# Optimization experiments

Hardware: AMD Instinct MI355X
Metric: run time of the kernel (lower is better)

## Reference

```python
import math
import jax, jax.numpy as jnp
import numpy as np

N_HEADS = 8
GROUPS = 32
EPS = 1e-5


def setup_inputs() -> dict:
    key = jax.random.key(0)
    ks = jax.random.split(key, 4)
    B, C, H, W = 8, 512, 32, 32
    x = jax.random.normal(ks[0], (B, C, H, W), dtype=jnp.float32)
    gn_scale = jnp.ones((C,), dtype=jnp.float32)
    gn_bias = jnp.zeros((C,), dtype=jnp.float32)
    # small init so softmax logits stay in a sane range (original zero-inits
    # proj_out; we use small random weights so the output is non-trivial)
    qkv_w = jax.random.normal(ks[1], (3 * C, C), dtype=jnp.float32) * 0.02
    qkv_b = jnp.zeros((3 * C,), dtype=jnp.float32)
    proj_w = jax.random.normal(ks[2], (C, C), dtype=jnp.float32) * 0.02
    proj_b = jnp.zeros((C,), dtype=jnp.float32)
    return {"x": x, "gn_scale": gn_scale, "gn_bias": gn_bias,
            "qkv_w": qkv_w, "qkv_b": qkv_b,
            "proj_w": proj_w, "proj_b": proj_b}


def reference(x, gn_scale, gn_bias, qkv_w, qkv_b, proj_w, proj_b):
    b, c, H, W = x.shape
    L = H * W
    xr = x.reshape(b, c, L)

    # GroupNorm32: normalize in fp32 over (channels_per_group, L)
    xf = xr.astype(jnp.float32).reshape(b, GROUPS, -1)
    mu = xf.mean(axis=-1, keepdims=True)
    var = xf.var(axis=-1, keepdims=True)
    xn = ((xf - mu) * jax.lax.rsqrt(var + EPS)).reshape(b, c, L)
    xn = (xn * gn_scale[:, None] + gn_bias[:, None]).astype(x.dtype)

    # 1x1 conv QKV projection: [b, 3C, L]
    qkv = jnp.einsum('oc,bcl->bol', qkv_w, xn) + qkv_b[:, None]

    # QKVAttentionLegacy: split 3C axis as (heads, 3*ch)
    ch = c // N_HEADS
    qkv = qkv.reshape(b * N_HEADS, 3 * ch, L)
    q, k, v = qkv[:, :ch], qkv[:, ch:2 * ch], qkv[:, 2 * ch:]
    scale = 1.0 / math.sqrt(math.sqrt(ch))
    w = jnp.einsum('bct,bcs->bts', q * scale, k * scale)  # [b*h, L, L]
    w = jax.nn.softmax(w.astype(jnp.float32), axis=-1).astype(qkv.dtype)
    a = jnp.einsum('bts,bcs->bct', w, v).reshape(b, c, L)

    # 1x1 conv output projection + residual
    h = jnp.einsum('oc,bcl->bol', proj_w, a) + proj_b[:, None]
    return (xr + h).reshape(b, c, H, W)
```

## Files before the change

### kernel.cpp

```cpp
#include <hip/hip_runtime.h>
#include <hip/hip_bf16.h>

typedef __attribute__((ext_vector_type(8))) short v8s;
typedef __attribute__((ext_vector_type(8))) unsigned short u16x8;
typedef __attribute__((ext_vector_type(4))) float v4f;
typedef __attribute__((ext_vector_type(16))) float f32x16;

#define MFMA16(a, b, c) __builtin_amdgcn_mfma_f32_16x16x32_bf16((a), (b), (c), 0, 0, 0)
#define MFMA32(a, b, c) __builtin_amdgcn_mfma_f32_32x32x16_bf16((a), (b), (c), 0, 0, 0)

#define GLL16(g, l)                                                        \
  __builtin_amdgcn_global_load_lds(                                        \
      (const __attribute__((address_space(1))) unsigned int*)(g),          \
      (__attribute__((address_space(3))) unsigned int*)(l), 16, 0, 0)

#if __has_builtin(__builtin_amdgcn_exp2f)
__device__ __forceinline__ float exp2n(float x) { return __builtin_amdgcn_exp2f(x); }
#else
__device__ __forceinline__ float exp2n(float x) {
  float r; asm("v_exp_f32 %0, %1" : "=v"(r) : "v"(x)); return r;
}
#endif

__device__ __forceinline__ unsigned short f2bf(float f) {
  union { float f; unsigned u; } v; v.f = f;
  unsigned r = v.u + 0x7fffu + ((v.u >> 16) & 1u);
  return (unsigned short)(r >> 16);
}

__device__ __forceinline__ unsigned cvtpk(float lo, float hi) {
  unsigned r;
  asm("v_cvt_pk_bf16_f32 %0, %1, %2" : "=v"(r) : "v"(lo), "v"(hi));
  return r;
}
__device__ __forceinline__ void pl32swap(unsigned& a, unsigned& b) {
  asm("v_permlane32_swap_b32 %0, %1" : "+v"(a), "+v"(b));
}

__global__ __launch_bounds__(256) void cvt_gn_kernel(const float* __restrict__ in0,
                                                     unsigned short* __restrict__ out0,
                                                     const float* __restrict__ in1,
                                                     unsigned short* __restrict__ out1,
                                                     int n0, int n1,
                                                     const float* __restrict__ x,
                                                     const float* __restrict__ gsc,
                                                     const float* __restrict__ gbi,
                                                     unsigned short* __restrict__ xnT) {
  __shared__ __align__(16) float xsf[16384];
  if (blockIdx.x < 1024) {
    int i = blockIdx.x * 256 + threadIdx.x;
    const float* in; unsigned short* out;
    if (i < n0) { in = in0; out = out0; }
    else        { i -= n0; if (i >= n1) return; in = in1; out = out1; }
    float4 v = ((const float4*)in)[i];
    ushort4 o;
    o.x = f2bf(v.x); o.y = f2bf(v.y); o.z = f2bf(v.z); o.w = f2bf(v.w);
    ((ushort4*)out)[i] = o;
    return;
  }
  const int bg = blockIdx.x - 1024;
  const int b = bg >> 5, g = bg & 31;
  const int tid = threadIdx.x;
  const float4* xp4 = (const float4*)(x + (size_t)bg * 16384);
  float4* xs4 = (float4*)xsf;
  float s = 0.f, ss = 0.f;
  #pragma unroll
  for (int k = 0; k < 16; ++k) {
    const int i = k * 256 + tid;
    float4 v = xp4[i];
    xs4[i] = v;
    s  += (v.x + v.y) + (v.z + v.w);
    ss += (v.x * v.x + v.y * v.y) + (v.z * v.z + v.w * v.w);
  }
  #pragma unroll
  for (int d = 1; d < 64; d <<= 1) { s += __shfl_xor(s, d); ss += __shfl_xor(ss, d); }
  __syncthreads();
  float save = 0.f;
  if (tid < 10) save = xsf[tid];
  __syncthreads();
  if ((tid & 63) == 0) { xsf[(tid >> 6) * 2] = s; xsf[(tid >> 6) * 2 + 1] = ss; }
  __syncthreads();
  if (tid == 0) {
    const float S  = xsf[0] + xsf[2] + xsf[4] + xsf[6];
    const float SS = xsf[1] + xsf[3] + xsf[5] + xsf[7];
    const float mu  = S * (1.f / 16384.f);
    const float var = SS * (1.f / 16384.f) - mu * mu;
    xsf[8] = mu; xsf[9] = rsqrtf(var + 1e-5f);
  }
  __syncthreads();
  const float mu = xsf[8], rs = xsf[9];
  __syncthreads();
  if (tid < 10) xsf[tid] = save;
  __syncthreads();
  float scv[16], biv[16];
  #pragma unroll
  for (int j = 0; j < 16; ++j) {
    scv[j] = gsc[g * 16 + j] * rs;
    biv[j] = gbi[g * 16 + j] - mu * scv[j];
  }
  unsigned short* dp = xnT + (size_t)b * 1024 * 512 + g * 16;
  #pragma unroll
  for (int k = 0; k < 4; ++k) {
    const int l = k * 256 + tid;
    u16x8 o0, o1;
    #pragma unroll
    for (int j = 0; j < 8; ++j) o0[j] = f2bf(xsf[j * 1024 + l] * scv[j] + biv[j]);
    #pragma unroll
    for (int j = 0; j < 8; ++j) o1[j] = f2bf(xsf[(8 + j) * 1024 + l] * scv[8 + j] + biv[8 + j]);
    *(u16x8*)(dp + (size_t)l * 512)     = o0;
    *(u16x8*)(dp + (size_t)l * 512 + 8) = o1;
  }
}

template <bool QKV, int NT>
__global__ __launch_bounds__(256) void gemm_kernel(
    const unsigned short* __restrict__ A,
    const unsigned short* __restrict__ BT,
    const float* __restrict__ bias,
    const float* __restrict__ xres,
    float* __restrict__ outf,
    unsigned short* __restrict__ qT,
    unsigned short* __restrict__ kT,
    unsigned short* __restrict__ vO) {
  constexpr int K = 512;
  constexpr int NFR = NT / 32;
  constexpr int NJOB = 16 + NT / 8;
  const int n0 = blockIdx.x * NT, m0 = blockIdx.y * 128, b = blockIdx.z;
  const unsigned short* Bp = BT + (size_t)b * 1024 * K;

  __shared__ __align__(16) unsigned short As[128][64];
  __shared__ __align__(16) unsigned short Bs[NT][64];

  const int tid = threadIdx.x, lane = tid & 63, w = tid >> 6;
  const int quad = lane >> 4, l15 = lane & 15;
  const int wm = (w >> 1) * 64, wn = (w & 1) * (NT / 2);
  const int srow = lane >> 3;
  const int scol = ((lane & 7) ^ srow) * 8;
  const int ck0 = ((quad ^ (l15 & 7)) * 8);
  const int ck1 = ck0 ^ 32;
  const unsigned short* Asf = &As[0][0];
  const unsigned short* Bsf = &Bs[0][0];

  v4f acc[4][NFR];
  #pragma unroll
  for (int i = 0; i < 4; ++i)
    #pragma unroll
    for (int j = 0; j < NFR; ++j) acc[i][j] = (v4f){0.f, 0.f, 0.f, 0.f};

  for (int kk = 0; kk < K; kk += 64) {
    __syncthreads();
    #pragma unroll
    for (int jj = 0; jj < NJOB / 4; ++jj) {
      const int job = w * (NJOB / 4) + jj;
      if (job < 16) {
        GLL16(A + (size_t)(m0 + job * 8 + srow) * K + kk + scol, &As[job * 8][0]);
      } else {
        const int j2 = job - 16;
        GLL16(Bp + (size_t)(n0 + j2 * 8 + srow) * K + kk + scol, &Bs[j2 * 8][0]);
      }
    }
    __syncthreads();
    #pragma unroll
    for (int h = 0; h < 2; ++h) {
      const int ck = h ? ck1 : ck0;
      v8s af[4], bf[NFR];
      #pragma unroll
      for (int mt = 0; mt < 4; ++mt) af[mt] = *(const v8s*)(Asf + (wm + mt * 16 + l15) * 64 + ck);
      #pragma unroll
      for (int nt = 0; nt < NFR; ++nt) bf[nt] = *(const v8s*)(Bsf + (wn + nt * 16 + l15) * 64 + ck);
      #pragma unroll
      for (int mt = 0; mt < 4; ++mt)
        #pragma unroll
        for (int nt = 0; nt < NFR; ++nt)
          acc[mt][nt] = MFMA16(af[mt], bf[nt], acc[mt][nt]);
    }
  }

  if (QKV) {
    const int bh8 = b * 8;
    const float cs = 0.18033688011112042f;
    #pragma unroll
    for (int mt = 0; mt < 4; ++mt) {
      const int m4 = m0 + wm + mt * 16 + quad * 4;
      const int h = m4 / 192;
      const int rr = m4 - h * 192;
      const int part = rr >> 6;
      const int ch = rr & 63;
      const float b0 = bias[m4], b1 = bias[m4 + 1], b2 = bias[m4 + 2], b3 = bias[m4 + 3];
      #pragma unroll
      for (int nt = 0; nt < NFR; ++nt) {
        const int n = n0 + wn + nt * 16 + l15;
        v4f a = acc[mt][nt];
        const float v0 = a[0] + b0, v1 = a[1] + b1, v2 = a[2] + b2, v3 = a[3] + b3;
        if (part == 0) {
          ushort4 st4;
          st4.x = f2bf(v0 * cs); st4.y = f2bf(v1 * cs);
          st4.z = f2bf(v2 * cs); st4.w = f2bf(v3 * cs);
          *(ushort4*)(qT + ((size_t)(bh8 + h) * 1024 + n) * 64 + ch) = st4;
        } else if (part == 1) {
          ushort4 st4;
          st4.x = f2bf(v0); st4.y = f2bf(v1); st4.z = f2bf(v2); st4.w = f2bf(v3);
          *(ushort4*)(kT + ((size_t)(bh8 + h) * 1024 + n) * 64 + ch) = st4;
        } else {
          unsigned short* dp = vO + ((size_t)(bh8 + h) * 64 + ch) * 1024 + n;
          dp[0] = f2bf(v0); dp[1024] = f2bf(v1); dp[2048] = f2bf(v2); dp[3072] = f2bf(v3);
        }
      }
    }
  } else {
    #pragma unroll
    for (int mt = 0; mt < 4; ++mt) {
      const int m4 = m0 + wm + mt * 16 + quad * 4;
      const float b0 = bias[m4], b1 = bias[m4 + 1], b2 = bias[m4 + 2], b3 = bias[m4 + 3];
      #pragma unroll
      for (int nt = 0; nt < NFR; ++nt) {
        const int n = n0 + wn + nt * 16 + l15;
        const size_t i0 = ((size_t)b * 512 + m4) * 1024 + n;
        outf[i0]        = xres[i0]        + acc[mt][nt][0] + b0;
        outf[i0 + 1024] = xres[i0 + 1024] + acc[mt][nt][1] + b1;
        outf[i0 + 2048] = xres[i0 + 2048] + acc[mt][nt][2] + b2;
        outf[i0 + 3072] = xres[i0 + 3072] + acc[mt][nt][3] + b3;
      }
    }
  }
}

__global__ __launch_bounds__(256) void attn_kernel(const unsigned short* __restrict__ qT,
                                                   const unsigned short* __restrict__ kT,
                                                   const unsigned short* __restrict__ vv,
                                                   unsigned short* __restrict__ aT) {
  const int bh = blockIdx.x;
  const int t0 = blockIdx.y * 128;
  const unsigned short* qb = qT + (size_t)bh * 1024 * 64;
  const unsigned short* kb = kT + (size_t)bh * 1024 * 64;
  const unsigned short* vb = vv + (size_t)bh * 64 * 1024;

  __shared__ __align__(16) unsigned short Ks[2][128][64];
  __shared__ __align__(16) unsigned short Vs[2][2][64][64];

  const int tid = threadIdx.x, w = tid >> 6, lane = tid & 63;
  const int l31 = lane & 31, h = lane >> 5;
  const int srow = lane >> 3;
  const int scol = ((lane & 7) ^ srow) * 8;

  #pragma unroll
  for (int jj = 0; jj < 4; ++jj) {
    const int seg = w * 4 + jj;
    GLL16(qb + (size_t)(t0 + seg * 8 + srow) * 64 + scol, &Ks[0][0][0] + seg * 8 * 64);
  }
  __syncthreads();
  v8s qf[4];
  {
    const int row = w * 32 + l31;
    const unsigned short* qr = &Ks[0][0][0] + row * 64;
    const int rx = row & 7;
    #pragma unroll
    for (int kb2 = 0; kb2 < 4; ++kb2)
      qf[kb2] = *(const v8s*)(qr + ((kb2 * 2 + h) ^ rx) * 8);
  }
  __syncthreads();

  #pragma unroll
  for (int jj = 0; jj < 8; ++jj) {
    const int j = w * 8 + jj;
    if (j < 16) {
      GLL16(kb + (size_t)(j * 8 + srow) * 64 + scol, &Ks[0][j * 8][0]);
    } else {
      const int j2 = j - 16, hf = j2 >> 3, cg = (j2 & 7) * 8;
      GLL16(vb + (size_t)(cg + srow) * 1024 + hf * 64 + scol, &Vs[0][hf][cg][0]);
    }
  }

  f32x16 o[2];
  #pragma unroll
  for (int cb = 0; cb < 2; ++cb)
    #pragma unroll
    for (int r = 0; r < 16; ++r) o[cb][r] = 0.f;
  float lsum = 0.f;

  for (int it = 0; it < 8; ++it) {
    __syncthreads();
    if (it + 1 < 8) {
      const int s1 = (it + 1) * 128, bp1 = (it + 1) & 1;
      #pragma unroll
      for (int jj = 0; jj < 8; ++jj) {
        const int j = w * 8 + jj;
        if (j < 16) {
          GLL16(kb + (size_t)(s1 + j * 8 + srow) * 64 + scol, &Ks[bp1][j * 8][0]);
        } else {
          const int j2 = j - 16, hf = j2 >> 3, cg = (j2 & 7) * 8;
          GLL16(vb + (size_t)(cg + srow) * 1024 + s1 + hf * 64 + scol,
                &Vs[bp1][hf][cg][0]);
        }
      }
    }
    const int buf = it & 1;

    #pragma unroll
    for (int hf = 0; hf < 2; ++hf) {
      const unsigned short* Kb = &Ks[buf][hf * 64][0];
      const unsigned short* Vb = &Vs[buf][hf][0][0];

      v8s kf[2][4], vf[2][4];
      #pragma unroll
      for (int sb = 0; sb < 2; ++sb) {
        const int row = sb * 32 + l31, rx = row & 7;
        const unsigned short* kr = Kb + row * 64;
        #pragma unroll
        for (int kb2 = 0; kb2 < 4; ++kb2)
          kf[sb][kb2] = *(const v8s*)(kr + ((kb2 * 2 + h) ^ rx) * 8);
      }
      #pragma unroll
      for (int cb = 0; cb < 2; ++cb) {
        const int row = cb * 32 + l31, rx = row & 7;
        const unsigned short* vr = Vb + row * 64;
        #pragma unroll
        for (int i = 0; i < 4; ++i)
          vf[cb][i] = *(const v8s*)(vr + ((i * 2 + h) ^ rx) * 8);
      }

      #pragma unroll
      for (int sb = 0; sb < 2; ++sb) {
        f32x16 sa = {0.f,0.f,0.f,0.f,0.f,0.f,0.f,0.f,0.f,0.f,0.f,0.f,0.f,0.f,0.f,0.f};
        #pragma unroll
        for (int kb2 = 0; kb2 < 4; ++kb2)
          sa = MFMA32(kf[sb][kb2], qf[kb2], sa);
        float p[16]; float rsum = 0.f;
        #pragma unroll
        for (int r = 0; r < 16; ++r) { p[r] = exp2n(sa[r]); rsum += p[r]; }
        lsum += rsum;
        unsigned c0 = cvtpk(p[0], p[1]),  c1 = cvtpk(p[2], p[3]);
        unsigned c2 = cvtpk(p[4], p[5]),  c3 = cvtpk(p[6], p[7]);
        pl32swap(c0, c2); pl32swap(c1, c3);
        unsigned c4 = cvtpk(p[8], p[9]),  c5 = cvtpk(p[10], p[11]);
        unsigned c6 = cvtpk(p[12], p[13]), c7 = cvtpk(p[14], p[15]);
        pl32swap(c4, c6); pl32swap(c5, c7);
        union { v8s v; unsigned u[4]; } pa0, pa1;
        pa0.u[0] = c0; pa0.u[1] = c1; pa0.u[2] = c2; pa0.u[3] = c3;
        pa1.u[0] = c4; pa1.u[1] = c5; pa1.u[2] = c6; pa1.u[3] = c7;
        #pragma unroll
        for (int cb = 0; cb < 2; ++cb) {
          o[cb] = MFMA32(pa0.v, vf[cb][sb * 2 + 0], o[cb]);
          o[cb] = MFMA32(pa1.v, vf[cb][sb * 2 + 1], o[cb]);
        }
      }
    }
  }

  const int b = bh >> 3, hd = bh & 7;
  lsum += __shfl_xor(lsum, 32);
  #pragma unroll
  for (int r = 0; r < 16; ++r) {
    const int trow = (r & 3) + 8 * (r >> 2) + 4 * h;
    const float inv = 1.0f / __shfl(lsum, trow);
    const int t = t0 + w * 32 + trow;
    unsigned short* dst = aT + ((size_t)b * 1024 + t) * 512 + hd * 64;
    dst[l31]      = f2bf(o[0][r] * inv);
    dst[32 + l31] = f2bf(o[1][r] * inv);
  }
}

extern "C" void kernel_launch(void* const* d_in, const int* in_sizes, int n_in,
                              void* d_out, int out_size, void* d_ws, size_t ws_size,
                              hipStream_t stream) {
  const float* x    = (const float*)d_in[0];
  const float* gsc  = (const float*)d_in[1];
  const float* gbi  = (const float*)d_in[2];
  const float* qkvw = (const float*)d_in[3];
  const float* qkvb = (const float*)d_in[4];
  const float* pjw  = (const float*)d_in[5];
  const float* pjb  = (const float*)d_in[6];
  float* out = (float*)d_out;

  unsigned short* ws  = (unsigned short*)d_ws;
  unsigned short* qw  = ws;
  unsigned short* pw  = qw + 786432;
  unsigned short* xnT = pw + 262144 + 1024;
  unsigned short* qT  = xnT + 4194304;
  unsigned short* kT  = qT + 4194304;
  unsigned short* vv  = kT + 4194304;
  unsigned short* aT  = vv + 4194304;

  cvt_gn_kernel<<<dim3(1280), dim3(256), 0, stream>>>(qkvw, qw, pjw, pw, 196608, 65536,
                                                      x, gsc, gbi, xnT);
  gemm_kernel<true, 128><<<dim3(8, 12, 8), dim3(256), 0, stream>>>(
      qw, xnT, qkvb, nullptr, nullptr, qT, kT, vv);
  attn_kernel<<<dim3(64, 8), dim3(256), 0, stream>>>(qT, kT, vv, aT);
  gemm_kernel<false, 64><<<dim3(16, 4, 8), dim3(256), 0, stream>>>(
      pw, aT, pjb, x, out, nullptr, nullptr, nullptr);
}
```

Baseline: 142.5 us.

## Use 512-thread attention blocks with a 4-slot LDS ring and 3-deep prefetch

The attention kernel now runs 8 waves per block covering 256 query rows, so each K/V tile loaded into LDS is shared by twice as many query rows. The K/V stream moves from a double buffer of 128-key tiles to a 4-slot ring of 64-key tiles, prefetched three tiles ahead. Explicit vmcnt waits and raw s_barriers replace __syncthreads. This aims to hide global-load latency and halve K/V traffic per query, at the cost of fewer blocks (256) on the device and hand-tuned wait counts that must match the number of loads issued per wave.

```diff
diff --git a/kernel.cpp b/kernel.cpp
--- a/kernel.cpp
+++ b/kernel.cpp
@@ -225,18 +225,17 @@
   }
 }
 
-__global__ __launch_bounds__(256) void attn_kernel(const unsigned short* __restrict__ qT,
+__global__ __launch_bounds__(512) void attn_kernel(const unsigned short* __restrict__ qT,
                                                    const unsigned short* __restrict__ kT,
                                                    const unsigned short* __restrict__ vv,
                                                    unsigned short* __restrict__ aT) {
   const int bh = blockIdx.x;
-  const int t0 = blockIdx.y * 128;
+  const int t0 = blockIdx.y * 256;
   const unsigned short* qb = qT + (size_t)bh * 1024 * 64;
   const unsigned short* kb = kT + (size_t)bh * 1024 * 64;
   const unsigned short* vb = vv + (size_t)bh * 64 * 1024;
 
-  __shared__ __align__(16) unsigned short Ks[2][128][64];
-  __shared__ __align__(16) unsigned short Vs[2][2][64][64];
+  __shared__ __align__(16) unsigned short ring[4][2][64][64];
 
   const int tid = threadIdx.x, w = tid >> 6, lane = tid & 63;
   const int l31 = lane & 31, h = lane >> 5;
@@ -246,13 +245,13 @@
   #pragma unroll
   for (int jj = 0; jj < 4; ++jj) {
     const int seg = w * 4 + jj;
-    GLL16(qb + (size_t)(t0 + seg * 8 + srow) * 64 + scol, &Ks[0][0][0] + seg * 8 * 64);
+    GLL16(qb + (size_t)(t0 + seg * 8 + srow) * 64 + scol, &ring[0][0][0][0] + seg * 8 * 64);
   }
   __syncthreads();
   v8s qf[4];
   {
     const int row = w * 32 + l31;
-    const unsigned short* qr = &Ks[0][0][0] + row * 64;
+    const unsigned short* qr = &ring[0][0][0][0] + row * 64;
     const int rx = row & 7;
     #pragma unroll
     for (int kb2 = 0; kb2 < 4; ++kb2)
@@ -261,13 +260,17 @@
   __syncthreads();
 
   #pragma unroll
-  for (int jj = 0; jj < 8; ++jj) {
-    const int j = w * 8 + jj;
-    if (j < 16) {
-      GLL16(kb + (size_t)(j * 8 + srow) * 64 + scol, &Ks[0][j * 8][0]);
-    } else {
-      const int j2 = j - 16, hf = j2 >> 3, cg = (j2 & 7) * 8;
-      GLL16(vb + (size_t)(cg + srow) * 1024 + hf * 64 + scol, &Vs[0][hf][cg][0]);
+  for (int tt = 0; tt < 3; ++tt) {
+    const int s1 = tt * 64;
+    #pragma unroll
+    for (int jj = 0; jj < 2; ++jj) {
+      if (w < 4) {
+        const int rg = (w * 2 + jj) * 8;
+        GLL16(kb + (size_t)(s1 + rg + srow) * 64 + scol, &ring[tt][0][rg][0]);
+      } else {
+        const int cg = ((w - 4) * 2 + jj) * 8;
+        GLL16(vb + (size_t)(cg + srow) * 1024 + s1 + scol, &ring[tt][1][cg][0]);
+      }
     }
   }
 
@@ -278,71 +281,73 @@
     for (int r = 0; r < 16; ++r) o[cb][r] = 0.f;
   float lsum = 0.f;
 
-  for (int it = 0; it < 8; ++it) {
-    __syncthreads();
-    if (it + 1 < 8) {
-      const int s1 = (it + 1) * 128, bp1 = (it + 1) & 1;
-      #pragma unroll
-      for (int jj = 0; jj < 8; ++jj) {
-        const int j = w * 8 + jj;
-        if (j < 16) {
-          GLL16(kb + (size_t)(s1 + j * 8 + srow) * 64 + scol, &Ks[bp1][j * 8][0]);
+  #pragma unroll
+  for (int t = 0; t < 16; ++t) {
+    asm volatile("s_barrier" ::: "memory");
+    if (t + 3 < 16) {
+      const int s1 = (t + 3) * 64, sl = (t + 3) & 3;
+      #pragma unroll
+      for (int jj = 0; jj < 2; ++jj) {
+        if (w < 4) {
+          const int rg = (w * 2 + jj) * 8;
+          GLL16(kb + (size_t)(s1 + rg + srow) * 64 + scol, &ring[sl][0][rg][0]);
         } else {
-          const int j2 = j - 16, hf = j2 >> 3, cg = (j2 & 7) * 8;
-          GLL16(vb + (size_t)(cg + srow) * 1024 + s1 + hf * 64 + scol,
-                &Vs[bp1][hf][cg][0]);
+          const int cg = ((w - 4) * 2 + jj) * 8;
+          GLL16(vb + (size_t)(cg + srow) * 1024 + s1 + scol, &ring[sl][1][cg][0]);
         }
       }
     }
-    const int buf = it & 1;
-
-    #pragma unroll
-    for (int hf = 0; hf < 2; ++hf) {
-      const unsigned short* Kb = &Ks[buf][hf * 64][0];
-      const unsigned short* Vb = &Vs[buf][hf][0][0];
-
-      v8s kf[2][4], vf[2][4];
-      #pragma unroll
-      for (int sb = 0; sb < 2; ++sb) {
-        const int row = sb * 32 + l31, rx = row & 7;
-        const unsigned short* kr = Kb + row * 64;
-        #pragma unroll
-        for (int kb2 = 0; kb2 < 4; ++kb2)
-          kf[sb][kb2] = *(const v8s*)(kr + ((kb2 * 2 + h) ^ rx) * 8);
-      }
+    if (t < 13)       asm volatile("s_waitcnt vmcnt(6)" ::: "memory");
+    else if (t == 13) asm volatile("s_waitcnt vmcnt(4)" ::: "memory");
+    else if (t == 14) asm volatile("s_waitcnt vmcnt(2)" ::: "memory");
+    else              asm volatile("s_waitcnt vmcnt(0)" ::: "memory");
+    asm volatile("s_barrier" ::: "memory");
+
+    const int sl = t & 3;
+    const unsigned short* Kb = &ring[sl][0][0][0];
+    const unsigned short* Vb = &ring[sl][1][0][0];
+
+    v8s kf[2][4], vf[2][4];
+    #pragma unroll
+    for (int sb = 0; sb < 2; ++sb) {
+      const int row = sb * 32 + l31, rx = row & 7;
+      const unsigned short* kr = Kb + row * 64;
+      #pragma unroll
+      for (int kb2 = 0; kb2 < 4; ++kb2)
+        kf[sb][kb2] = *(const v8s*)(kr + ((kb2 * 2 + h) ^ rx) * 8);
+    }
+    #pragma unroll
+    for (int cb = 0; cb < 2; ++cb) {
+      const int row = cb * 32 + l31, rx = row & 7;
+      const unsigned short* vr = Vb + row * 64;
+      #pragma unroll
+      for (int i = 0; i < 4; ++i)
+        vf[cb][i] = *(const v8s*)(vr + ((i * 2 + h) ^ rx) * 8);
+    }
+
+    #pragma unroll
+    for (int sb = 0; sb < 2; ++sb) {
+      f32x16 sa = {0.f,0.f,0.f,0.f,0.f,0.f,0.f,0.f,0.f,0.f,0.f,0.f,0.f,0.f,0.f,0.f};
+      #pragma unroll
+      for (int kb2 = 0; kb2 < 4; ++kb2)
+        sa = MFMA32(kf[sb][kb2], qf[kb2], sa);
+      float p[16]; float rsum = 0.f;
+      #pragma unroll
+      for (int r = 0; r < 16; ++r) { p[r] = exp2n(sa[r]); rsum += p[r]; }
+      lsum += rsum;
+      unsigned c0 = cvtpk(p[0], p[1]),  c1 = cvtpk(p[2], p[3]);
+      unsigned c2 = cvtpk(p[4], p[5]),  c3 = cvtpk(p[6], p[7]);
+      pl32swap(c0, c2); pl32swap(c1, c3);
+      unsigned c4 = cvtpk(p[8], p[9]),  c5 = cvtpk(p[10], p[11]);
+      unsigned c6 = cvtpk(p[12], p[13]), c7 = cvtpk(p[14], p[15]);
+      pl32swap(c4, c6); pl32swap(c5, c7);
+      union { v8s v; unsigned u[4]; } pa0, pa1;
+      pa0.u[0] = c0; pa0.u[1] = c1; pa0.u[2] = c2; pa0.u[3] = c3;
+      pa1.u[0] = c4; pa1.u[1] = c5; pa1.u[2] = c6; pa1.u[3] = c7;
       #pragma unroll
       for (int cb = 0; cb < 2; ++cb) {
-        const int row = cb * 32 + l31, rx = row & 7;
-        const unsigned short* vr = Vb + row * 64;
-        #pragma unroll
-        for (int i = 0; i < 4; ++i)
-          vf[cb][i] = *(const v8s*)(vr + ((i * 2 + h) ^ rx) * 8);
-      }
-
-      #pragma unroll
-      for (int sb = 0; sb < 2; ++sb) {
-        f32x16 sa = {0.f,0.f,0.f,0.f,0.f,0.f,0.f,0.f,0.f,0.f,0.f,0.f,0.f,0.f,0.f,0.f};
-        #pragma unroll
-        for (int kb2 = 0; kb2 < 4; ++kb2)
-          sa = MFMA32(kf[sb][kb2], qf[kb2], sa);
-        float p[16]; float rsum = 0.f;
-        #pragma unroll
-        for (int r = 0; r < 16; ++r) { p[r] = exp2n(sa[r]); rsum += p[r]; }
-        lsum += rsum;
-        unsigned c0 = cvtpk(p[0], p[1]),  c1 = cvtpk(p[2], p[3]);
-        unsigned c2 = cvtpk(p[4], p[5]),  c3 = cvtpk(p[6], p[7]);
-        pl32swap(c0, c2); pl32swap(c1, c3);
-        unsigned c4 = cvtpk(p[8], p[9]),  c5 = cvtpk(p[10], p[11]);
-        unsigned c6 = cvtpk(p[12], p[13]), c7 = cvtpk(p[14], p[15]);
-        pl32swap(c4, c6); pl32swap(c5, c7);
-        union { v8s v; unsigned u[4]; } pa0, pa1;
-        pa0.u[0] = c0; pa0.u[1] = c1; pa0.u[2] = c2; pa0.u[3] = c3;
-        pa1.u[0] = c4; pa1.u[1] = c5; pa1.u[2] = c6; pa1.u[3] = c7;
-        #pragma unroll
-        for (int cb = 0; cb < 2; ++cb) {
-          o[cb] = MFMA32(pa0.v, vf[cb][sb * 2 + 0], o[cb]);
-          o[cb] = MFMA32(pa1.v, vf[cb][sb * 2 + 1], o[cb]);
-        }
+        o[cb] = MFMA32(pa0.v, vf[cb][sb * 2 + 0], o[cb]);
+        o[cb] = MFMA32(pa1.v, vf[cb][sb * 2 + 1], o[cb]);
       }
     }
   }
@@ -385,7 +390,7 @@
                                                       x, gsc, gbi, xnT);
   gemm_kernel<true, 128><<<dim3(8, 12, 8), dim3(256), 0, stream>>>(
       qw, xnT, qkvb, nullptr, nullptr, qT, kT, vv);
-  attn_kernel<<<dim3(64, 8), dim3(256), 0, stream>>>(qT, kT, vv, aT);
+  attn_kernel<<<dim3(64, 4), dim3(512), 0, stream>>>(qT, kT, vv, aT);
   gemm_kernel<false, 64><<<dim3(16, 4, 8), dim3(256), 0, stream>>>(
       pw, aT, pjb, x, out, nullptr, nullptr, nullptr);
 }
```

Measured after the change: 233.4 us. 63.8% more time.
